# Kernel tuning notes

Measured on AMD Instinct MI355X. Metric: run time of the kernel, lower is better.

Reference implementation:

```python
import jax, jax.numpy as jnp
import numpy as np

H = 128  # hidden_dim
COORD_CLAMP = 100.0


def _glorot(key, shape):
    fan_in, fan_out = shape[0], shape[1]
    lim = float(np.sqrt(6.0 / (fan_in + fan_out)))
    return jax.random.uniform(key, shape, jnp.float32, -lim, lim)


def setup_inputs() -> dict:
    key = jax.random.key(0)
    ks = jax.random.split(key, 20)
    B, N = 2, 512
    inp = {
        "h": jax.random.normal(ks[0], (B, N, H), jnp.float32),
        "pos": jax.random.normal(ks[1], (B, N, 3), jnp.float32),
        "vel": jax.random.normal(ks[2], (B, N, 3), jnp.float32),
        # edge_mlp: Linear(2H+2 -> H), SiLU, Linear(H -> H), SiLU
        "We1": _glorot(ks[3], (2 * H + 2, H)), "be1": jnp.zeros((H,), jnp.float32),
        "We2": _glorot(ks[4], (H, H)), "be2": jnp.zeros((H,), jnp.float32),
        # attention_mlp: Linear(H -> 1), Sigmoid
        "Wa": _glorot(ks[5], (H, 1)), "ba": jnp.zeros((1,), jnp.float32),
        # pos_mlp: Linear(H -> H), SiLU, Linear(H -> 1, no bias)
        "Wp1": _glorot(ks[6], (H, H)), "bp1": jnp.zeros((H,), jnp.float32),
        "Wp2": _glorot(ks[7], (H, 1)),
        # vel_mlp: Linear(H -> H), SiLU, Linear(H -> 1, no bias)
        "Wv1": _glorot(ks[8], (H, H)), "bv1": jnp.zeros((H,), jnp.float32),
        "Wv2": _glorot(ks[9], (H, 1)),
        # node_mlp: Linear(2H -> H), SiLU, Linear(H -> H)
        "Wn1": _glorot(ks[10], (2 * H, H)), "bn1": jnp.zeros((H,), jnp.float32),
        "Wn2": _glorot(ks[11], (H, H)), "bn2": jnp.zeros((H,), jnp.float32),
    }
    return inp


def reference(h, pos, vel, We1, be1, We2, be2, Wa, ba,
              Wp1, bp1, Wp2, Wv1, bv1, Wv2, Wn1, bn1, Wn2, bn2):
    B, N, _ = pos.shape
    # pairwise diffs: [B, N, N, 3]
    pos_diff = pos[:, :, None, :] - pos[:, None, :, :]
    vel_diff = vel[:, :, None, :] - vel[:, None, :, :]
    pos_dist_sq = jnp.sum(pos_diff ** 2, axis=-1, keepdims=True)  # [B,N,N,1]
    vel_dist_sq = jnp.sum(vel_diff ** 2, axis=-1, keepdims=True)
    h_i = jnp.broadcast_to(h[:, :, None, :], (B, N, N, H))
    h_j = jnp.broadcast_to(h[:, None, :, :], (B, N, N, H))
    edge_input = jnp.concatenate([h_i, h_j, pos_dist_sq, vel_dist_sq], axis=-1)  # [B,N,N,2H+2]
    # edge MLP
    m = jax.nn.silu(jnp.einsum('bijc,ch->bijh', edge_input, We1) + be1)
    m_ij = jax.nn.silu(jnp.einsum('bijh,hk->bijk', m, We2) + be2)
    # attention gate
    att = jax.nn.sigmoid(jnp.einsum('bijh,ho->bijo', m_ij, Wa) + ba)  # [B,N,N,1]
    m_ij = m_ij * att
    # tanh-weighted coordinate/velocity updates
    pos_w = jnp.tanh(jnp.einsum('bijh,ho->bijo', jax.nn.silu(jnp.einsum('bijh,hk->bijk', m_ij, Wp1) + bp1), Wp2))
    vel_w = jnp.tanh(jnp.einsum('bijh,ho->bijo', jax.nn.silu(jnp.einsum('bijh,hk->bijk', m_ij, Wv1) + bv1), Wv2))
    denom = jnp.float32(max(N - 1, 1))
    pos_update = jnp.sum(pos_diff * pos_w, axis=2) / denom  # [B,N,3]
    vel_update = jnp.sum(vel_diff * vel_w, axis=2) / denom
    pos_out = jnp.clip(pos + pos_update, -COORD_CLAMP, COORD_CLAMP)
    vel_out = jnp.clip(vel + vel_update, -COORD_CLAMP, COORD_CLAMP)
    # node update
    m_agg = jnp.sum(m_ij, axis=2)  # [B,N,H]
    node_input = jnp.concatenate([h, m_agg], axis=-1)  # [B,N,2H]
    h_out = jax.nn.silu(jnp.einsum('bnc,ch->bnh', node_input, Wn1) + bn1)
    h_out = jnp.einsum('bnh,hk->bnk', h_out, Wn2) + bn2
    h_out = h + h_out  # residual
    return (h_out, pos_out, vel_out)
```

## Files before the change

kernel.cpp:

```cpp
#include <hip/hip_runtime.h>
#include <hip/hip_bf16.h>

#define Hd 128
#define Nn 512
#define TJ 32
#define LSTRIDE 136

typedef __bf16 bf16x8 __attribute__((ext_vector_type(8)));
typedef float  floatx4 __attribute__((ext_vector_type(4)));

__device__ __forceinline__ float frcp(float x){ return __builtin_amdgcn_rcpf(x); }
__device__ __forceinline__ float fsilu(float x){ return x * frcp(1.f + __expf(-x)); }
__device__ __forceinline__ float fsigm(float x){ return frcp(1.f + __expf(-x)); }
__device__ __forceinline__ float ftanh(float x){ return 1.f - 2.f * frcp(__expf(2.f*x) + 1.f); }
__device__ __forceinline__ float rfl(float x){
  return __int_as_float(__builtin_amdgcn_readfirstlane(__float_as_int(x)));
}

__global__ __launch_bounds__(256) void prep(const float* __restrict__ h,
                                            const float* __restrict__ We1,
                                            const float* __restrict__ be1,
                                            const float* __restrict__ We2,
                                            const float* __restrict__ Wp1,
                                            const float* __restrict__ Wv1,
                                            float* __restrict__ A,
                                            float* __restrict__ Bm,
                                            __bf16* __restrict__ dst,
                                            float* __restrict__ zbase){
  if (blockIdx.x < 256){
    const int r0 = blockIdx.x * 4;
    const int k = threadIdx.x & 127, ch = threadIdx.x >> 7;
    __shared__ float hL[4][Hd];
    __shared__ float pa[2][4][Hd], pb[2][4][Hd];
    for (int idx = threadIdx.x; idx < 4*Hd; idx += 256)
      hL[idx >> 7][idx & 127] = h[r0*Hd + idx];
    __syncthreads();
    float a[4] = {0.f,0.f,0.f,0.f}, bb[4] = {0.f,0.f,0.f,0.f};
    const int cbase = ch*64;
    #pragma unroll 4
    for (int cc = 0; cc < 64; ++cc){
      const int c = cbase + cc;
      const float wa = We1[c*Hd + k];
      const float wb = We1[(c + Hd)*Hd + k];
      #pragma unroll
      for (int rr = 0; rr < 4; ++rr){
        a[rr]  += hL[rr][c] * wa;
        bb[rr] += hL[rr][c] * wb;
      }
    }
    #pragma unroll
    for (int rr = 0; rr < 4; ++rr){ pa[ch][rr][k] = a[rr]; pb[ch][rr][k] = bb[rr]; }
    __syncthreads();
    if (threadIdx.x < Hd){
      const float be = be1[k];
      #pragma unroll
      for (int rr = 0; rr < 4; ++rr){
        A[(r0+rr)*Hd + k]  = pa[0][rr][k] + pa[1][rr][k] + be;
        Bm[(r0+rr)*Hd + k] = pb[0][rr][k] + pb[1][rr][k];
      }
    }
  } else if (blockIdx.x < 280){
    const int blk = blockIdx.x - 256;
    const int which = blk >> 3, m = blk & 7;
    const float* src = (which == 0) ? We2 : (which == 1 ? Wp1 : Wv1);
    __bf16* d = dst + which * (Hd*Hd);
    #pragma unroll
    for (int it = 0; it < 8; ++it){
      const int sidx = m*2048 + it*256 + threadIdx.x;
      const int kk = sidx >> 7, cc = sidx & 127;
      const int s = kk >> 5, j = kk & 7;
      const int lane = ((kk >> 3) & 3)*16 + (cc & 15);
      const int n = cc >> 4;
      d[n*2048 + s*512 + lane*8 + j] = (__bf16)src[sidx];
    }
  } else {
    const int t0 = (blockIdx.x - 280)*256 + threadIdx.x;
    for (int idx = t0; idx < 137216; idx += 2048) zbase[idx] = 0.f;
  }
}

__device__ __forceinline__ void gemm_kloop(const __bf16* __restrict__ buf,
                                           const bf16x8* __restrict__ Bs,
                                           int w, int lane, int q, int l15,
                                           floatx4 acc[2][2]){
  const floatx4 zero = {0.f, 0.f, 0.f, 0.f};
  #pragma unroll
  for (int m = 0; m < 2; ++m){ acc[m][0] = zero; acc[m][1] = zero; }
  #pragma unroll
  for (int s = 0; s < 4; ++s){
    bf16x8 af[2];
    #pragma unroll
    for (int m = 0; m < 2; ++m)
      af[m] = *(const bf16x8*)&buf[(16*m + l15)*LSTRIDE + s*32 + q*8];
    const bf16x8 b0 = Bs[((2*w + 0)*4 + s)*64 + lane];
    const bf16x8 b1 = Bs[((2*w + 1)*4 + s)*64 + lane];
    #pragma unroll
    for (int m = 0; m < 2; ++m){
      acc[m][0] = __builtin_amdgcn_mfma_f32_16x16x32_bf16(af[m], b0, acc[m][0], 0, 0, 0);
      acc[m][1] = __builtin_amdgcn_mfma_f32_16x16x32_bf16(af[m], b1, acc[m][1], 0, 0, 0);
    }
  }
}

__device__ __forceinline__ float fold_reduce8(float pr[8], int lane){
  #pragma unroll
  for (int k = 0; k < 4; ++k){
    const float send = (lane & 1) ? pr[k] : pr[k+4];
    const float recv = __shfl_xor(send, 1, 64);
    pr[k] = ((lane & 1) ? pr[k+4] : pr[k]) + recv;
  }
  #pragma unroll
  for (int k = 0; k < 2; ++k){
    const float send = (lane & 2) ? pr[k] : pr[k+2];
    const float recv = __shfl_xor(send, 2, 64);
    pr[k] = ((lane & 2) ? pr[k+2] : pr[k]) + recv;
  }
  {
    const float send = (lane & 4) ? pr[0] : pr[1];
    const float recv = __shfl_xor(send, 4, 64);
    pr[0] = ((lane & 4) ? pr[1] : pr[0]) + recv;
  }
  pr[0] += __shfl_xor(pr[0], 8, 64);
  return pr[0];
}
__device__ __forceinline__ int bitrev3(int x){
  return ((x&1)<<2) | (x&2) | ((x&4)>>2);
}

__device__ __forceinline__ void wdot_epilogue(floatx4 acc[2][2],
                                              const float att[2][4],
                                              const float* __restrict__ biasL,
                                              const float* __restrict__ wG,
                                              int w, int lane, int q, int l15,
                                              float (*part)[TJ]){
  float pr[8];
  #pragma unroll
  for (int k = 0; k < 8; ++k) pr[k] = 0.f;
  const int c0 = 32*w + l15, c1 = c0 + 16;
  const float bb0 = biasL[c0], bb1 = biasL[c1];
  const float ww0 = wG[c0],    ww1 = wG[c1];
  #pragma unroll
  for (int m = 0; m < 2; ++m){
    #pragma unroll
    for (int r = 0; r < 4; ++r){
      pr[4*m + r] += fsilu(fmaf(att[m][r], acc[m][0][r], bb0)) * ww0;
      pr[4*m + r] += fsilu(fmaf(att[m][r], acc[m][1][r], bb1)) * ww1;
    }
  }
  const float v = fold_reduce8(pr, lane);
  if ((lane & 15) < 8){
    const int k = bitrev3(l15 & 7);
    part[w][16*(k >> 2) + 4*q + (k & 3)] = v;
  }
}

__global__ __launch_bounds__(256) void egnn_main(
    const float* __restrict__ pos, const float* __restrict__ vel,
    const float* __restrict__ We1, const float* __restrict__ be2,
    const float* __restrict__ Wa,  const float* __restrict__ ba,
    const float* __restrict__ bp1, const float* __restrict__ Wp2,
    const float* __restrict__ bv1, const float* __restrict__ Wv2,
    const float* __restrict__ A,   const float* __restrict__ Bm,
    const __bf16* __restrict__ Wsw,
    float* __restrict__ magg, float* __restrict__ posu, float* __restrict__ velu){

  const int t    = threadIdx.x;
  const int w    = t >> 6;
  const int lane = t & 63;
  const int q    = lane >> 4;
  const int l15  = lane & 15;
  const int node = blockIdx.x >> 1;
  const int half = blockIdx.x & 1;
  const int b    = node >> 9;

  __shared__ float AiL[Hd], wpL[Hd], wvL[Hd], be2L[Hd], bp1L[Hd], bv1L[Hd];
  __shared__ __align__(16) __bf16 bufm [TJ*LSTRIDE];
  __shared__ __align__(16) __bf16 bufij[TJ*LSTRIDE];
  __shared__ float partAtt[4][TJ], partP[4][TJ], partV[4][TJ];
  __shared__ float attL[TJ];

  if (t < Hd){
    AiL[t]  = A[node*Hd + t];
    wpL[t]  = We1[256*Hd + t];
    wvL[t]  = We1[257*Hd + t];
    be2L[t] = be2[t]; bp1L[t] = bp1[t]; bv1L[t] = bv1[t];
  }
  const float baV = ba[0];
  const float* pi = &pos[(size_t)node*3];
  const float* vi = &vel[(size_t)node*3];
  const float px = rfl(pi[0]), py = rfl(pi[1]), pz = rfl(pi[2]);
  const float ux = rfl(vi[0]), uy = rfl(vi[1]), uz = rfl(vi[2]);
  __syncthreads();

  const bf16x8* We2s = (const bf16x8*)(Wsw);
  const bf16x8* Wp1s = (const bf16x8*)(Wsw + Hd*Hd);
  const bf16x8* Wv1s = (const bf16x8*)(Wsw + 2*Hd*Hd);

  float accR[8];
  #pragma unroll
  for (int e = 0; e < 8; ++e) accR[e] = 0.f;

  for (int jt = 0; jt < (Nn/2)/TJ; ++jt){
    const int j0 = half*(Nn/2) + jt * TJ;

    {
      const int g  = t & 15;
      const int j2 = t >> 4;
      const floatx4 a0 = *(const floatx4*)&AiL[g*8];
      const floatx4 a1 = *(const floatx4*)&AiL[g*8 + 4];
      const floatx4 p0 = *(const floatx4*)&wpL[g*8];
      const floatx4 p1 = *(const floatx4*)&wpL[g*8 + 4];
      const floatx4 v0 = *(const floatx4*)&wvL[g*8];
      const floatx4 v1 = *(const floatx4*)&wvL[g*8 + 4];
      #pragma unroll
      for (int rr = 0; rr < 2; ++rr){
        const int j = j2 + rr*16;
        const int jg = j0 + j;
        const float* pj = &pos[(size_t)(b*Nn + jg)*3];
        const float* vj = &vel[(size_t)(b*Nn + jg)*3];
        const float dx = px - pj[0], dy = py - pj[1], dz = pz - pj[2];
        const float dp = dx*dx + dy*dy + dz*dz;
        const float ex = ux - vj[0], ey = uy - vj[1], ez = uz - vj[2];
        const float dv = ex*ex + ey*ey + ez*ez;
        const floatx4* Bp4 = (const floatx4*)&Bm[((size_t)(b*Nn + jg))*Hd + g*8];
        const floatx4 b0 = Bp4[0], b1 = Bp4[1];
        union { bf16x8 v; __hip_bfloat162 h2[4]; } o;
        float x[8];
        #pragma unroll
        for (int e = 0; e < 4; ++e){
          x[e]   = fsilu(a0[e] + b0[e] + dp*p0[e] + dv*v0[e]);
          x[4+e] = fsilu(a1[e] + b1[e] + dp*p1[e] + dv*v1[e]);
        }
        o.h2[0] = __float22bfloat162_rn(make_float2(x[0], x[1]));
        o.h2[1] = __float22bfloat162_rn(make_float2(x[2], x[3]));
        o.h2[2] = __float22bfloat162_rn(make_float2(x[4], x[5]));
        o.h2[3] = __float22bfloat162_rn(make_float2(x[6], x[7]));
        *(bf16x8*)&bufm[j*LSTRIDE + g*8] = o.v;
      }
    }
    __syncthreads();

    {
      floatx4 acc[2][2];
      gemm_kloop(bufm, We2s, w, lane, q, l15, acc);
      float aw[8];
      #pragma unroll
      for (int k = 0; k < 8; ++k) aw[k] = 0.f;
      const int c0 = 32*w + l15, c1 = c0 + 16;
      const float bb0 = be2L[c0], bb1 = be2L[c1];
      const float wa0 = Wa[c0],   wa1 = Wa[c1];
      #pragma unroll
      for (int m = 0; m < 2; ++m){
        #pragma unroll
        for (int r = 0; r < 4; ++r){
          const int row = 16*m + 4*q + r;
          const float sv0 = fsilu(acc[m][0][r] + bb0);
          const float sv1 = fsilu(acc[m][1][r] + bb1);
          bufij[row*LSTRIDE + c0] = (__bf16)sv0;
          bufij[row*LSTRIDE + c1] = (__bf16)sv1;
          aw[4*m + r] += sv0*wa0 + sv1*wa1;
        }
      }
      const float v = fold_reduce8(aw, lane);
      if (l15 < 8){
        const int k = bitrev3(l15);
        partAtt[w][16*(k >> 2) + 4*q + (k & 3)] = v;
      }
    }
    __syncthreads();

    {
      const int rowX = (16*(l15 & 3) + 4*q + (l15 >> 2)) & (TJ - 1);
      const float attv = fsigm(partAtt[0][rowX] + partAtt[1][rowX] +
                               partAtt[2][rowX] + partAtt[3][rowX] + baV);
      if (w == 3 && (l15 & 3) < 2) attL[rowX] = attv;
      floatx4 acc[2][2];
      gemm_kloop(bufij, Wp1s, w, lane, q, l15, acc);
      float att[2][4];
      #pragma unroll
      for (int m = 0; m < 2; ++m)
        #pragma unroll
        for (int r = 0; r < 4; ++r)
          att[m][r] = __shfl(attv, 16*q + 4*r + m, 64);
      wdot_epilogue(acc, att, bp1L, Wp2, w, lane, q, l15, partP);
      gemm_kloop(bufij, Wv1s, w, lane, q, l15, acc);
      wdot_epilogue(acc, att, bv1L, Wv2, w, lane, q, l15, partV);
    }
    __syncthreads();

    if (w == 0){
      if (lane < TJ){
        const int jg = j0 + lane;
        const float* pj = &pos[(size_t)(b*Nn + jg)*3];
        const float s4 = partP[0][lane] + partP[1][lane] + partP[2][lane] + partP[3][lane];
        const float pw = ftanh(s4);
        accR[0] += (px - pj[0]) * pw;
        accR[1] += (py - pj[1]) * pw;
        accR[2] += (pz - pj[2]) * pw;
      }
    } else if (w == 1){
      if (lane < TJ){
        const int jg = j0 + lane;
        const float* vj = &vel[(size_t)(b*Nn + jg)*3];
        const float s4 = partV[0][lane] + partV[1][lane] + partV[2][lane] + partV[3][lane];
        const float vw = ftanh(s4);
        accR[0] += (ux - vj[0]) * vw;
        accR[1] += (uy - vj[1]) * vw;
        accR[2] += (uz - vj[2]) * vw;
      }
    } else {
      const int sg   = (w - 2)*8 + (lane & 7);
      const int jsub = lane >> 3;
      #pragma unroll
      for (int jj = 0; jj < 4; ++jj){
        const int j = jj*8 + jsub;
        const float aj = attL[j];
        const bf16x8 v = *(const bf16x8*)&bufij[j*LSTRIDE + sg*8];
        #pragma unroll
        for (int e = 0; e < 8; ++e) accR[e] += aj * (float)v[e];
      }
    }
  }

  if (w == 0 || w == 1){
    float v0 = accR[0], v1 = accR[1], v2 = accR[2];
    #pragma unroll
    for (int off = 1; off < 64; off <<= 1){
      v0 += __shfl_xor(v0, off, 64);
      v1 += __shfl_xor(v1, off, 64);
      v2 += __shfl_xor(v2, off, 64);
    }
    if (lane == 0){
      float* dst = (w == 0) ? &posu[node*3] : &velu[node*3];
      atomicAdd(&dst[0], v0);
      atomicAdd(&dst[1], v1);
      atomicAdd(&dst[2], v2);
    }
  } else {
    const int sg = (w - 2)*8 + (lane & 7);
    #pragma unroll
    for (int off = 8; off < 64; off <<= 1){
      #pragma unroll
      for (int e = 0; e < 8; ++e) accR[e] += __shfl_xor(accR[e], off, 64);
    }
    if ((lane >> 3) == 0){
      #pragma unroll
      for (int e = 0; e < 8; ++e)
        atomicAdd(&magg[node*Hd + sg*8 + e], accR[e]);
    }
  }
}

__global__ __launch_bounds__(256) void egnn_final(
    const float* __restrict__ h, const float* __restrict__ pos, const float* __restrict__ vel,
    const float* __restrict__ Wn1, const float* __restrict__ bn1,
    const float* __restrict__ Wn2, const float* __restrict__ bn2,
    const float* __restrict__ magg, const float* __restrict__ posu,
    const float* __restrict__ velu, float* __restrict__ out){
  const int row = blockIdx.x;
  const int t = threadIdx.x;
  const int k = t & 127, ch = t >> 7;
  __shared__ float ni[2*Hd];
  __shared__ float p1[2][Hd], t1[Hd];
  ni[t] = (t < Hd) ? h[row*Hd + t] : magg[row*Hd + (t - Hd)];
  __syncthreads();
  {
    float a0=0.f,a1=0.f,a2=0.f,a3=0.f;
    const int cb = ch*Hd;
    #pragma unroll 8
    for (int cc = 0; cc < Hd; cc += 4){
      a0 += ni[cb+cc+0] * Wn1[(cb+cc+0)*Hd + k];
      a1 += ni[cb+cc+1] * Wn1[(cb+cc+1)*Hd + k];
      a2 += ni[cb+cc+2] * Wn1[(cb+cc+2)*Hd + k];
      a3 += ni[cb+cc+3] * Wn1[(cb+cc+3)*Hd + k];
    }
    p1[ch][k] = (a0+a1)+(a2+a3);
  }
  __syncthreads();
  if (t < Hd) t1[t] = fsilu(p1[0][t] + p1[1][t] + bn1[t]);
  __syncthreads();
  {
    float a0=0.f,a1=0.f,a2=0.f,a3=0.f;
    const int cb = ch*64;
    #pragma unroll 8
    for (int cc = 0; cc < 64; cc += 4){
      a0 += t1[cb+cc+0] * Wn2[(cb+cc+0)*Hd + k];
      a1 += t1[cb+cc+1] * Wn2[(cb+cc+1)*Hd + k];
      a2 += t1[cb+cc+2] * Wn2[(cb+cc+2)*Hd + k];
      a3 += t1[cb+cc+3] * Wn2[(cb+cc+3)*Hd + k];
    }
    p1[ch][k] = (a0+a1)+(a2+a3);
  }
  __syncthreads();
  if (t < Hd){
    out[row*Hd + t] = ni[t] + p1[0][t] + p1[1][t] + bn2[t];
  } else if (t < Hd + 3){
    const int d = t - Hd;
    const float v = pos[row*3 + d] + posu[row*3 + d] * (1.f/511.f);
    out[2*Nn*Hd + row*3 + d] = fminf(fmaxf(v, -100.f), 100.f);
  } else if (t < Hd + 6){
    const int d = t - Hd - 3;
    const float v = vel[row*3 + d] + velu[row*3 + d] * (1.f/511.f);
    out[2*Nn*Hd + 2*Nn*3 + row*3 + d] = fminf(fmaxf(v, -100.f), 100.f);
  }
}

extern "C" void kernel_launch(void* const* d_in, const int* in_sizes, int n_in,
                              void* d_out, int out_size, void* d_ws, size_t ws_size,
                              hipStream_t stream){
  const float* h   = (const float*)d_in[0];
  const float* pos = (const float*)d_in[1];
  const float* vel = (const float*)d_in[2];
  const float* We1 = (const float*)d_in[3];
  const float* be1 = (const float*)d_in[4];
  const float* We2 = (const float*)d_in[5];
  const float* be2 = (const float*)d_in[6];
  const float* Wa  = (const float*)d_in[7];
  const float* ba  = (const float*)d_in[8];
  const float* Wp1 = (const float*)d_in[9];
  const float* bp1 = (const float*)d_in[10];
  const float* Wp2 = (const float*)d_in[11];
  const float* Wv1 = (const float*)d_in[12];
  const float* bv1 = (const float*)d_in[13];
  const float* Wv2 = (const float*)d_in[14];
  const float* Wn1 = (const float*)d_in[15];
  const float* bn1 = (const float*)d_in[16];
  const float* Wn2 = (const float*)d_in[17];
  const float* bn2 = (const float*)d_in[18];

  float* ws = (float*)d_ws;
  float*  A    = ws;
  float*  Bmm  = ws + 131072;
  float*  magg = ws + 262144;
  float*  posu = ws + 393216;
  float*  velu = ws + 396288;
  __bf16* Wsw  = (__bf16*)(ws + 399360);

  prep      <<<dim3(288),  dim3(256), 0, stream>>>(h, We1, be1, We2, Wp1, Wv1,
                                                   A, Bmm, Wsw, magg);
  egnn_main <<<dim3(2048), dim3(256), 0, stream>>>(pos, vel, We1, be2, Wa, ba, bp1, Wp2,
                                                   bv1, Wv2, A, Bmm, Wsw, magg, posu, velu);
  egnn_final<<<dim3(1024), dim3(256), 0, stream>>>(h, pos, vel, Wn1, bn1, Wn2, bn2,
                                                   magg, posu, velu, (float*)d_out);
}
```

Baseline: 247.4 us.

## Transpose MFMA operand roles so epilogue reductions use cheap cross-lane shuffles

The edge GEMMs now pass the weight tile as the A operand and the edge activations as B, so each lane's accumulator holds four consecutive hidden features for one edge. The dot-product epilogues for attention, pos and vel weights then reduce within a lane plus two xor-shuffles, replacing the 8-way fold reduction and bit-reversed scatter. The attention broadcast shuffles go away, and bufij stores become 4-wide bf16 vector writes. Small weight vectors (Wa, Wp2, Wv2) are also staged in shared memory. This relies on the pre-swizzled weight layout being equally valid as the A operand, which may need care for correctness.

```diff
diff --git a/kernel.cpp b/kernel.cpp
--- a/kernel.cpp
+++ b/kernel.cpp
@@ -7,6 +7,7 @@
 #define LSTRIDE 136
 
 typedef __bf16 bf16x8 __attribute__((ext_vector_type(8)));
+typedef __bf16 bf16x4 __attribute__((ext_vector_type(4)));
 typedef float  floatx4 __attribute__((ext_vector_type(4)));
 
 __device__ __forceinline__ float frcp(float x){ return __builtin_amdgcn_rcpf(x); }
@@ -79,78 +80,52 @@
   }
 }
 
-__device__ __forceinline__ void gemm_kloop(const __bf16* __restrict__ buf,
-                                           const bf16x8* __restrict__ Bs,
-                                           int w, int lane, int q, int l15,
-                                           floatx4 acc[2][2]){
+__device__ __forceinline__ void gemm_kloopT(const __bf16* __restrict__ buf,
+                                            const bf16x8* __restrict__ Ws,
+                                            int w, int lane, int q, int l15,
+                                            floatx4 acc[2][2]){
   const floatx4 zero = {0.f, 0.f, 0.f, 0.f};
   #pragma unroll
   for (int m = 0; m < 2; ++m){ acc[m][0] = zero; acc[m][1] = zero; }
   #pragma unroll
   for (int s = 0; s < 4; ++s){
-    bf16x8 af[2];
-    #pragma unroll
-    for (int m = 0; m < 2; ++m)
-      af[m] = *(const bf16x8*)&buf[(16*m + l15)*LSTRIDE + s*32 + q*8];
-    const bf16x8 b0 = Bs[((2*w + 0)*4 + s)*64 + lane];
-    const bf16x8 b1 = Bs[((2*w + 1)*4 + s)*64 + lane];
-    #pragma unroll
-    for (int m = 0; m < 2; ++m){
-      acc[m][0] = __builtin_amdgcn_mfma_f32_16x16x32_bf16(af[m], b0, acc[m][0], 0, 0, 0);
-      acc[m][1] = __builtin_amdgcn_mfma_f32_16x16x32_bf16(af[m], b1, acc[m][1], 0, 0, 0);
-    }
-  }
-}
-
-__device__ __forceinline__ float fold_reduce8(float pr[8], int lane){
+    bf16x8 bf[2];
+    #pragma unroll
+    for (int n = 0; n < 2; ++n)
+      bf[n] = *(const bf16x8*)&buf[(16*n + l15)*LSTRIDE + s*32 + q*8];
+    const bf16x8 a0 = Ws[((2*w + 0)*4 + s)*64 + lane];
+    const bf16x8 a1 = Ws[((2*w + 1)*4 + s)*64 + lane];
+    #pragma unroll
+    for (int n = 0; n < 2; ++n){
+      acc[0][n] = __builtin_amdgcn_mfma_f32_16x16x32_bf16(a0, bf[n], acc[0][n], 0, 0, 0);
+      acc[1][n] = __builtin_amdgcn_mfma_f32_16x16x32_bf16(a1, bf[n], acc[1][n], 0, 0, 0);
+    }
+  }
+}
+
+__device__ __forceinline__ void wdotT(floatx4 acc[2][2], float att0, float att1,
+                                      const float* __restrict__ biasL,
+                                      const float* __restrict__ w2L,
+                                      int w, int lane, int q, int l15,
+                                      float (*part)[TJ]){
+  const int fb0 = 32*w + 4*q, fb1 = fb0 + 16;
+  const floatx4 bb0 = *(const floatx4*)&biasL[fb0];
+  const floatx4 bb1 = *(const floatx4*)&biasL[fb1];
+  const floatx4 w0  = *(const floatx4*)&w2L[fb0];
+  const floatx4 w1  = *(const floatx4*)&w2L[fb1];
+  float p0 = 0.f, p1 = 0.f;
   #pragma unroll
-  for (int k = 0; k < 4; ++k){
-    const float send = (lane & 1) ? pr[k] : pr[k+4];
-    const float recv = __shfl_xor(send, 1, 64);
-    pr[k] = ((lane & 1) ? pr[k+4] : pr[k]) + recv;
-  }
-  #pragma unroll
-  for (int k = 0; k < 2; ++k){
-    const float send = (lane & 2) ? pr[k] : pr[k+2];
-    const float recv = __shfl_xor(send, 2, 64);
-    pr[k] = ((lane & 2) ? pr[k+2] : pr[k]) + recv;
-  }
-  {
-    const float send = (lane & 4) ? pr[0] : pr[1];
-    const float recv = __shfl_xor(send, 4, 64);
-    pr[0] = ((lane & 4) ? pr[1] : pr[0]) + recv;
-  }
-  pr[0] += __shfl_xor(pr[0], 8, 64);
-  return pr[0];
-}
-__device__ __forceinline__ int bitrev3(int x){
-  return ((x&1)<<2) | (x&2) | ((x&4)>>2);
-}
-
-__device__ __forceinline__ void wdot_epilogue(floatx4 acc[2][2],
-                                              const float att[2][4],
-                                              const float* __restrict__ biasL,
-                                              const float* __restrict__ wG,
-                                              int w, int lane, int q, int l15,
-                                              float (*part)[TJ]){
-  float pr[8];
-  #pragma unroll
-  for (int k = 0; k < 8; ++k) pr[k] = 0.f;
-  const int c0 = 32*w + l15, c1 = c0 + 16;
-  const float bb0 = biasL[c0], bb1 = biasL[c1];
-  const float ww0 = wG[c0],    ww1 = wG[c1];
-  #pragma unroll
-  for (int m = 0; m < 2; ++m){
-    #pragma unroll
-    for (int r = 0; r < 4; ++r){
-      pr[4*m + r] += fsilu(fmaf(att[m][r], acc[m][0][r], bb0)) * ww0;
-      pr[4*m + r] += fsilu(fmaf(att[m][r], acc[m][1][r], bb1)) * ww1;
-    }
-  }
-  const float v = fold_reduce8(pr, lane);
-  if ((lane & 15) < 8){
-    const int k = bitrev3(l15 & 7);
-    part[w][16*(k >> 2) + 4*q + (k & 3)] = v;
+  for (int r = 0; r < 4; ++r){
+    p0 += fsilu(fmaf(att0, acc[0][0][r], bb0[r])) * w0[r];
+    p0 += fsilu(fmaf(att0, acc[1][0][r], bb1[r])) * w1[r];
+    p1 += fsilu(fmaf(att1, acc[0][1][r], bb0[r])) * w0[r];
+    p1 += fsilu(fmaf(att1, acc[1][1][r], bb1[r])) * w1[r];
+  }
+  p0 += __shfl_xor(p0, 16, 64); p0 += __shfl_xor(p0, 32, 64);
+  p1 += __shfl_xor(p1, 16, 64); p1 += __shfl_xor(p1, 32, 64);
+  if (lane < 16){
+    part[w][l15]      = p0;
+    part[w][16 + l15] = p1;
   }
 }
 
@@ -173,7 +148,8 @@
   const int half = blockIdx.x & 1;
   const int b    = node >> 9;
 
-  __shared__ float AiL[Hd], wpL[Hd], wvL[Hd], be2L[Hd], bp1L[Hd], bv1L[Hd];
+  __shared__ float AiL[Hd], wpL[Hd], wvL[Hd];
+  __shared__ float be2L[Hd], bp1L[Hd], bv1L[Hd], WaL[Hd], Wp2L[Hd], Wv2L[Hd];
   __shared__ __align__(16) __bf16 bufm [TJ*LSTRIDE];
   __shared__ __align__(16) __bf16 bufij[TJ*LSTRIDE];
   __shared__ float partAtt[4][TJ], partP[4][TJ], partV[4][TJ];
@@ -184,6 +160,7 @@
     wpL[t]  = We1[256*Hd + t];
     wvL[t]  = We1[257*Hd + t];
     be2L[t] = be2[t]; bp1L[t] = bp1[t]; bv1L[t] = bv1[t];
+    WaL[t]  = Wa[t];  Wp2L[t] = Wp2[t]; Wv2L[t] = Wv2[t];
   }
   const float baV = ba[0];
   const float* pi = &pos[(size_t)node*3];
@@ -242,49 +219,52 @@
 
     {
       floatx4 acc[2][2];
-      gemm_kloop(bufm, We2s, w, lane, q, l15, acc);
-      float aw[8];
-      #pragma unroll
-      for (int k = 0; k < 8; ++k) aw[k] = 0.f;
-      const int c0 = 32*w + l15, c1 = c0 + 16;
-      const float bb0 = be2L[c0], bb1 = be2L[c1];
-      const float wa0 = Wa[c0],   wa1 = Wa[c1];
-      #pragma unroll
-      for (int m = 0; m < 2; ++m){
+      gemm_kloopT(bufm, We2s, w, lane, q, l15, acc);
+      const int fb0 = 32*w + 4*q, fb1 = fb0 + 16;
+      const floatx4 be0 = *(const floatx4*)&be2L[fb0];
+      const floatx4 be1 = *(const floatx4*)&be2L[fb1];
+      const floatx4 wa0 = *(const floatx4*)&WaL[fb0];
+      const floatx4 wa1 = *(const floatx4*)&WaL[fb1];
+      float aw[2];
+      #pragma unroll
+      for (int n = 0; n < 2; ++n){
+        const int j = 16*n + l15;
+        float s0[4], s1[4];
         #pragma unroll
         for (int r = 0; r < 4; ++r){
-          const int row = 16*m + 4*q + r;
-          const float sv0 = fsilu(acc[m][0][r] + bb0);
-          const float sv1 = fsilu(acc[m][1][r] + bb1);
-          bufij[row*LSTRIDE + c0] = (__bf16)sv0;
-          bufij[row*LSTRIDE + c1] = (__bf16)sv1;
-          aw[4*m + r] += sv0*wa0 + sv1*wa1;
+          s0[r] = fsilu(acc[0][n][r] + be0[r]);
+          s1[r] = fsilu(acc[1][n][r] + be1[r]);
         }
-      }
-      const float v = fold_reduce8(aw, lane);
-      if (l15 < 8){
-        const int k = bitrev3(l15);
-        partAtt[w][16*(k >> 2) + 4*q + (k & 3)] = v;
+        aw[n] = s0[0]*wa0[0] + s0[1]*wa0[1] + s0[2]*wa0[2] + s0[3]*wa0[3]
+              + s1[0]*wa1[0] + s1[1]*wa1[1] + s1[2]*wa1[2] + s1[3]*wa1[3];
+        union { bf16x4 v; __hip_bfloat162 h2[2]; } p0k, p1k;
+        p0k.h2[0] = __float22bfloat162_rn(make_float2(s0[0], s0[1]));
+        p0k.h2[1] = __float22bfloat162_rn(make_float2(s0[2], s0[3]));
+        p1k.h2[0] = __float22bfloat162_rn(make_float2(s1[0], s1[1]));
+        p1k.h2[1] = __float22bfloat162_rn(make_float2(s1[2], s1[3]));
+        *(bf16x4*)&bufij[j*LSTRIDE + fb0] = p0k.v;
+        *(bf16x4*)&bufij[j*LSTRIDE + fb1] = p1k.v;
+      }
+      aw[0] += __shfl_xor(aw[0], 16, 64); aw[0] += __shfl_xor(aw[0], 32, 64);
+      aw[1] += __shfl_xor(aw[1], 16, 64); aw[1] += __shfl_xor(aw[1], 32, 64);
+      if (lane < 16){
+        partAtt[w][l15]      = aw[0];
+        partAtt[w][16 + l15] = aw[1];
       }
     }
     __syncthreads();
 
     {
-      const int rowX = (16*(l15 & 3) + 4*q + (l15 >> 2)) & (TJ - 1);
-      const float attv = fsigm(partAtt[0][rowX] + partAtt[1][rowX] +
-                               partAtt[2][rowX] + partAtt[3][rowX] + baV);
-      if (w == 3 && (l15 & 3) < 2) attL[rowX] = attv;
+      const float att0 = fsigm(partAtt[0][l15] + partAtt[1][l15] +
+                               partAtt[2][l15] + partAtt[3][l15] + baV);
+      const float att1 = fsigm(partAtt[0][16+l15] + partAtt[1][16+l15] +
+                               partAtt[2][16+l15] + partAtt[3][16+l15] + baV);
+      if (w == 0 && lane < 16){ attL[l15] = att0; attL[16 + l15] = att1; }
       floatx4 acc[2][2];
-      gemm_kloop(bufij, Wp1s, w, lane, q, l15, acc);
-      float att[2][4];
-      #pragma unroll
-      for (int m = 0; m < 2; ++m)
-        #pragma unroll
-        for (int r = 0; r < 4; ++r)
-          att[m][r] = __shfl(attv, 16*q + 4*r + m, 64);
-      wdot_epilogue(acc, att, bp1L, Wp2, w, lane, q, l15, partP);
-      gemm_kloop(bufij, Wv1s, w, lane, q, l15, acc);
-      wdot_epilogue(acc, att, bv1L, Wv2, w, lane, q, l15, partV);
+      gemm_kloopT(bufij, Wp1s, w, lane, q, l15, acc);
+      wdotT(acc, att0, att1, bp1L, Wp2L, w, lane, q, l15, partP);
+      gemm_kloopT(bufij, Wv1s, w, lane, q, l15, acc);
+      wdotT(acc, att0, att1, bv1L, Wv2L, w, lane, q, l15, partV);
     }
     __syncthreads();
 
```

New measurement: 233.4 us. 5.6% less time.
